# Kernel tuning notes

Hardware: AMD Instinct MI355X
Metric: run time of the kernel (lower is better)

## Reference

```python
import jax, jax.numpy as jnp
import numpy as np

N_NODES = 2048
N_EDGES = 8192
EDGE_DIM = 10
EDGE_HIDDEN = 32
HID = 160


def nnconv(x, edge_index, edge_attr, w1, b1, w2, b2, root, bias):
    """PyG-style NNConv with aggr='mean'.
    x: [N, HID], edge_attr: [E, EDGE_DIM], edge_index: [2, E] (src, dst).
    Per-edge weight W_e = MLP(e) reshaped to [HID, HID]; message = x[src] @ W_e,
    mean-aggregated at dst, plus root transform and bias.
    """
    n = x.shape[0]
    h = jax.nn.relu(edge_attr @ w1 + b1)                     # [E, EDGE_HIDDEN]
    W = (h @ w2 + b2).reshape(-1, HID, HID)                  # [E, HID, HID]
    src, dst = edge_index[0], edge_index[1]
    msg = jnp.einsum('ei,eio->eo', x[src], W)                # [E, HID]
    summed = jax.ops.segment_sum(msg, dst, num_segments=n)   # [N, HID]
    cnt = jax.ops.segment_sum(jnp.ones((msg.shape[0],), x.dtype), dst,
                              num_segments=n)
    aggr = summed / jnp.maximum(cnt, 1.0)[:, None]           # mean; 0 for isolated
    return aggr + x @ root + bias


def setup_inputs() -> dict:
    key = jax.random.key(0)
    ks = jax.random.split(key, 16)
    s = 1.0 / np.sqrt(HID)
    se = 1.0 / np.sqrt(EDGE_DIM)
    sh = 1.0 / np.sqrt(EDGE_HIDDEN)
    inp = {
        'x': jax.random.normal(ks[0], (N_NODES, HID), jnp.float32),
        'edge_attr': jax.random.uniform(ks[1], (N_EDGES, EDGE_DIM), jnp.float32),
        # conv1 (subgraph_conv1) params
        'w1_a': jax.random.normal(ks[2], (EDGE_DIM, EDGE_HIDDEN), jnp.float32) * se,
        'b1_a': jnp.zeros((EDGE_HIDDEN,), jnp.float32),
        'w2_a': jax.random.normal(ks[3], (EDGE_HIDDEN, HID * HID), jnp.float32) * sh,
        'b2_a': jnp.zeros((HID * HID,), jnp.float32),
        'root_a': jax.random.normal(ks[4], (HID, HID), jnp.float32) * s,
        'bias_a': jnp.zeros((HID,), jnp.float32),
        # conv2 (subgraph_conv2, applied twice) params
        'w1_b': jax.random.normal(ks[5], (EDGE_DIM, EDGE_HIDDEN), jnp.float32) * se,
        'b1_b': jnp.zeros((EDGE_HIDDEN,), jnp.float32),
        'w2_b': jax.random.normal(ks[6], (EDGE_HIDDEN, HID * HID), jnp.float32) * sh,
        'b2_b': jnp.zeros((HID * HID,), jnp.float32),
        'root_b': jax.random.normal(ks[7], (HID, HID), jnp.float32) * s,
        'bias_b': jnp.zeros((HID,), jnp.float32),
        'edge_index': jax.random.randint(ks[8], (2, N_EDGES), 0, N_NODES, jnp.int64),
    }
    return inp


def reference(x, edge_attr, w1_a, b1_a, w2_a, b2_a, root_a, bias_a,
              w1_b, b1_b, w2_b, b2_b, root_b, bias_b, edge_index):
    # subgraph_conv1 -> ReLU -> subgraph_conv2 -> ReLU -> subgraph_conv2
    h = jax.nn.relu(nnconv(x, edge_index, edge_attr,
                           w1_a, b1_a, w2_a, b2_a, root_a, bias_a))
    h = jax.nn.relu(nnconv(h, edge_index, edge_attr,
                           w1_b, b1_b, w2_b, b2_b, root_b, bias_b))
    h = nnconv(h, edge_index, edge_attr,
               w1_b, b1_b, w2_b, b2_b, root_b, bias_b)
    return h
```

## Files before the change

kernel.cpp:

```cpp
#include <hip/hip_runtime.h>

#define NN 2048
#define NE 8192
#define ED 10
#define EH 32
#define HID 160
#define KT 5440
#define KS 10
#define KSL 544
#define MT 32
#define APAD 552
#define NNH (NN * HID)

typedef __attribute__((ext_vector_type(8))) short short8;
typedef __attribute__((ext_vector_type(4))) float f32x4;
typedef unsigned int u32;

__device__ __forceinline__ ushort f2bf(float v) {
    u32 u = __float_as_uint(v);
    u += 0x7FFF + ((u >> 16) & 1);
    return (ushort)(u >> 16);
}
__device__ __forceinline__ u32 packbf(float lo, float hi) {
    return ((u32)f2bf(hi) << 16) | f2bf(lo);
}
__device__ __forceinline__ void gl2lds16(const ushort* g, ushort* l) {
    __builtin_amdgcn_global_load_lds(
        (const __attribute__((address_space(1))) u32*)g,
        (__attribute__((address_space(3))) u32*)l, 16, 0, 0);
}

__global__ __launch_bounds__(256) void k_prep(
        const float* __restrict__ ea,
        const float* __restrict__ w1a, const float* __restrict__ b1a,
        const float* __restrict__ w1b, const float* __restrict__ b1b,
        float* __restrict__ ha, float* __restrict__ hb,
        const float* __restrict__ w2a, const float* __restrict__ b2a,
        const float* __restrict__ roota,
        const float* __restrict__ w2b, const float* __restrict__ b2b,
        const float* __restrict__ rootb,
        ushort* __restrict__ WcA, ushort* __restrict__ WcB,
        const float* __restrict__ biasa, const float* __restrict__ biasb,
        float* __restrict__ xacc0, float* __restrict__ xacc1,
        float* __restrict__ outb,
        const int* __restrict__ ei, int* __restrict__ doff,
        int* __restrict__ degg, float* __restrict__ dinv,
        int* __restrict__ delist) {
    __shared__ __align__(16) char smem[21760];
    int b = blockIdx.x, t = threadIdx.x;

    if (b < 512) {
        int set = b >> 8, rel = b & 255;
        const float* w1 = set ? w1b : w1a;
        const float* b1 = set ? b1b : b1a;
        float* h = set ? hb : ha;
        int idx = rel * 1024 + t * 4;
        int e = idx >> 5, j0 = idx & 31;
        float o4[4];
#pragma unroll
        for (int u = 0; u < 4; ++u) {
            float acc = b1[j0 + u];
#pragma unroll
            for (int i = 0; i < ED; ++i) acc += ea[e * ED + i] * w1[i * EH + j0 + u];
            o4[u] = fmaxf(acc, 0.f);
        }
        *(float4*)&h[idx] = *(const float4*)o4;
        return;
    }
    if (b < 672) {
        int rel = b - 512;
        int set = rel / 80, i0 = (rel % 80) * 2;
        u32 (*tile)[34] = (u32(*)[34])smem;
        const float* w2 = set ? w2b : w2a;
        const float* b2 = set ? b2b : b2a;
        const float* root = set ? rootb : roota;
        ushort* W = set ? WcB : WcA;
        if (t < HID) {
#pragma unroll
            for (int di = 0; di < 2; ++di) {
                int i = i0 + di;
#pragma unroll
                for (int p = 0; p < 16; ++p) {
                    float v0 = w2[(size_t)(2 * p) * 25600 + i * HID + t];
                    float v1 = w2[(size_t)(2 * p + 1) * 25600 + i * HID + t];
                    tile[t][di * 17 + p] = packbf(v0, v1);
                }
                tile[t][di * 17 + 16] = packbf(b2[i * HID + t], root[i * HID + t]);
            }
        }
        __syncthreads();
        u32* dst = (u32*)W;
        for (int w = t; w < 5440; w += 256) {
            int o = w / 34, j = w - o * 34;
            dst[(size_t)o * 2720 + i0 * 17 + j] = tile[o][j];
        }
        return;
    }
    if (b < 912) {
        int jb = b - 672;
        int buf = jb / 80, rel = jb % 80;
        float* dst = buf == 0 ? xacc0 : (buf == 1 ? xacc1 : outb);
        const float* bias = buf == 0 ? biasa : biasb;
        int base = rel * 4096 + t * 16;
#pragma unroll
        for (int k = 0; k < 4; ++k) {
            int idx = base + k * 4;
            *(float4*)&dst[idx] = *(const float4*)&bias[idx % HID];
        }
        return;
    }
    int* deg = (int*)smem;
    int* cur = deg + NN;
    int* part = cur + NN;
    for (int i = t; i < NN; i += 256) deg[i] = 0;
    __syncthreads();
    for (int e = t; e < NE; e += 256) atomicAdd(&deg[ei[NE + e]], 1);
    __syncthreads();
    int loc[8], s = 0;
#pragma unroll
    for (int i = 0; i < 8; ++i) { loc[i] = s; s += deg[t * 8 + i]; }
    part[t] = s;
    __syncthreads();
    int tot = s;
    for (int st = 1; st < 256; st <<= 1) {
        int v = (t >= st) ? part[t - st] : 0;
        __syncthreads();
        part[t] += v;
        __syncthreads();
    }
    int base = part[t] - tot;
#pragma unroll
    for (int i = 0; i < 8; ++i) {
        int d = t * 8 + i;
        doff[d] = base + loc[i];
        cur[d] = base + loc[i];
        degg[d] = deg[d];
        dinv[d] = 1.0f / fmaxf((float)deg[d], 1.0f);
    }
    __syncthreads();
    for (int e = t; e < NE; e += 256) {
        int d = ei[NE + e];
        int p = atomicAdd(&cur[d], 1);
        delist[p] = e;
    }
}

__global__ __launch_bounds__(256) void k_layer(
        const float* __restrict__ xin, int dorelu,
        const float* __restrict__ h, const ushort* __restrict__ wc,
        const int* __restrict__ ei, const int* __restrict__ doff,
        const int* __restrict__ degg, const float* __restrict__ dinv,
        const int* __restrict__ delist, float* __restrict__ obuf) {
    __shared__ __align__(16) ushort sA[MT * APAD];
    __shared__ __align__(16) ushort sB[2][160 * 32];
    int t = threadIdx.x;
    int bm = blockIdx.x, ks = blockIdx.y;
    int d0 = bm * MT, i0 = ks * 16;

    auto stage = [&](int buf, int c) {
        size_t k0 = (size_t)ks * KSL + c * 32;
#pragma unroll
        for (int q = 0; q < 2; ++q) {
            int s = t + q * 256;
            int row = s >> 2;
            int lkq = (s & 3) ^ ((row >> 1) & 3);
            gl2lds16(&wc[(size_t)row * KT + k0 + lkq * 8], &sB[buf][s * 8]);
        }
        if (t < 128) {
            int s = t + 512;
            int row = s >> 2;
            int lkq = (s & 3) ^ ((row >> 1) & 3);
            gl2lds16(&wc[(size_t)row * KT + k0 + lkq * 8], &sB[buf][s * 8]);
        }
    };
    stage(0, 0);

    int il = t & 15, i = i0 + il;
    int dA = d0 + (t >> 4), dB = dA + 16;
    auto ldx = [&](int node) {
        float v = xin[node * HID + i];
        return dorelu ? fmaxf(v, 0.f) : v;
    };
    float accA[33], accB[33];
#pragma unroll
    for (int q = 0; q < 33; ++q) { accA[q] = 0.f; accB[q] = 0.f; }

    int aLo = doff[dA], aHi = aLo + degg[dA];
    for (int o = aLo; o < aHi; ++o) {
        int e = delist[o];
        float xs = ldx(ei[e]);
        const float4* hp = (const float4*)&h[(size_t)e * EH];
#pragma unroll
        for (int q8 = 0; q8 < 8; ++q8) {
            float4 hv = hp[q8];
            accA[q8 * 4 + 0] += hv.x * xs;
            accA[q8 * 4 + 1] += hv.y * xs;
            accA[q8 * 4 + 2] += hv.z * xs;
            accA[q8 * 4 + 3] += hv.w * xs;
        }
        accA[32] += xs;
    }
    int bLo = doff[dB], bHi = bLo + degg[dB];
    for (int o = bLo; o < bHi; ++o) {
        int e = delist[o];
        float xs = ldx(ei[e]);
        const float4* hp = (const float4*)&h[(size_t)e * EH];
#pragma unroll
        for (int q8 = 0; q8 < 8; ++q8) {
            float4 hv = hp[q8];
            accB[q8 * 4 + 0] += hv.x * xs;
            accB[q8 * 4 + 1] += hv.y * xs;
            accB[q8 * 4 + 2] += hv.z * xs;
            accB[q8 * 4 + 3] += hv.w * xs;
        }
        accB[32] += xs;
    }
    float rootA = ldx(dA), rootB = ldx(dB);

    {
        float diA = dinv[dA], diB = dinv[dB];
        u32* pa = (u32*)&sA[(t >> 4) * APAD + il * 34];
        u32* pb = (u32*)&sA[((t >> 4) + 16) * APAD + il * 34];
#pragma unroll
        for (int p = 0; p < 16; ++p) {
            pa[p] = packbf(accA[2 * p] * diA, accA[2 * p + 1] * diA);
            pb[p] = packbf(accB[2 * p] * diB, accB[2 * p + 1] * diB);
        }
        pa[16] = packbf(accA[32] * diA, rootA);
        pb[16] = packbf(accB[32] * diB, rootB);
    }
    __syncthreads();

    int wid = t >> 6, lane = t & 63;
    int wm = (wid >> 1) * 16, wn = (wid & 1) * 80;
    int lr = lane & 15, lk = lane >> 4;
    f32x4 acc[5];
#pragma unroll
    for (int j = 0; j < 5; ++j) acc[j] = (f32x4){0.f, 0.f, 0.f, 0.f};

    for (int c = 0; c < 17; ++c) {
        int cur = c & 1;
        if (c + 1 < 17) stage(cur ^ 1, c + 1);
        short8 av = *(const short8*)&sA[(wm + lr) * APAD + c * 32 + lk * 8];
        short8 bv[5];
#pragma unroll
        for (int nt = 0; nt < 5; ++nt) {
            int row = wn + nt * 16 + lr;
            bv[nt] = *(const short8*)&sB[cur][row * 32 +
                                             (lk ^ ((row >> 1) & 3)) * 8];
        }
#pragma unroll
        for (int nt = 0; nt < 5; ++nt)
            acc[nt] = __builtin_amdgcn_mfma_f32_16x16x32_bf16(av, bv[nt], acc[nt], 0, 0, 0);
        __syncthreads();
    }

#pragma unroll
    for (int nt = 0; nt < 5; ++nt) {
        int n = wn + nt * 16 + lr;
        int m0 = d0 + wm + lk * 4;
#pragma unroll
        for (int r = 0; r < 4; ++r)
            unsafeAtomicAdd(&obuf[(size_t)(m0 + r) * HID + n], acc[nt][r]);
    }
}

extern "C" void kernel_launch(void* const* d_in, const int* in_sizes, int n_in,
                              void* d_out, int out_size, void* d_ws, size_t ws_size,
                              hipStream_t stream) {
    const float* x     = (const float*)d_in[0];
    const float* ea    = (const float*)d_in[1];
    const float* w1a   = (const float*)d_in[2];
    const float* b1a   = (const float*)d_in[3];
    const float* w2a   = (const float*)d_in[4];
    const float* b2a   = (const float*)d_in[5];
    const float* roota = (const float*)d_in[6];
    const float* biasa = (const float*)d_in[7];
    const float* w1b   = (const float*)d_in[8];
    const float* b1b   = (const float*)d_in[9];
    const float* w2b   = (const float*)d_in[10];
    const float* b2b   = (const float*)d_in[11];
    const float* rootb = (const float*)d_in[12];
    const float* biasb = (const float*)d_in[13];
    const int*   ei    = (const int*)d_in[14];
    float* out = (float*)d_out;

    char* p = (char*)d_ws;
    float* xacc0 = (float*)p;  p += (size_t)NNH * 4;
    float* xacc1 = (float*)p;  p += (size_t)NNH * 4;
    ushort* WcA  = (ushort*)p; p += (size_t)HID * KT * 2;
    ushort* WcB  = (ushort*)p; p += (size_t)HID * KT * 2;
    float* h_a   = (float*)p;  p += (size_t)NE * EH * 4;
    float* h_b   = (float*)p;  p += (size_t)NE * EH * 4;
    int* doff    = (int*)p;    p += NN * 4;
    int* degg    = (int*)p;    p += NN * 4;
    float* dinv  = (float*)p;  p += NN * 4;
    int* delist  = (int*)p;    p += NE * 4;

    k_prep<<<913, 256, 0, stream>>>(ea, w1a, b1a, w1b, b1b, h_a, h_b,
                                    w2a, b2a, roota, w2b, b2b, rootb, WcA, WcB,
                                    biasa, biasb, xacc0, xacc1, out,
                                    ei, doff, degg, dinv, delist);

    dim3 lg(NN / MT, KS);
    k_layer<<<lg, 256, 0, stream>>>(x, 0, h_a, WcA,
                                    ei, doff, degg, dinv, delist, xacc0);
    k_layer<<<lg, 256, 0, stream>>>(xacc0, 1, h_b, WcB,
                                    ei, doff, degg, dinv, delist, xacc1);
    k_layer<<<lg, 256, 0, stream>>>(xacc1, 1, h_b, WcB,
                                    ei, doff, degg, dinv, delist, out);
}
```

Baseline: 227.3 us.

## Replace atomic split-K output with partial buffers and last-block reduction epilogue

Each split-K block now writes its partial tile to a per-split buffer instead of doing float atomics. A per-row-block counter picks the last-arriving block, which sums the partials, adds the bias, applies ReLU and writes the layer output. This removes the bias-init pass from the prep kernel and the ReLU on loads in the next layer. Other changes: B tiles are read directly from global memory instead of being staged through LDS with double buffering, the edge list stores (edge, src) pairs to drop one indirection, and launch bounds now request 4 blocks per SM. The trade is extra partial-buffer traffic, a fence-and-counter sync, and B loads that are no longer staged through LDS.

New measurement: 474.2 us. 109% more time.

```diff
diff --git a/kernel.cpp b/kernel.cpp
--- a/kernel.cpp
+++ b/kernel.cpp
@@ -24,11 +24,6 @@
 __device__ __forceinline__ u32 packbf(float lo, float hi) {
     return ((u32)f2bf(hi) << 16) | f2bf(lo);
 }
-__device__ __forceinline__ void gl2lds16(const ushort* g, ushort* l) {
-    __builtin_amdgcn_global_load_lds(
-        (const __attribute__((address_space(1))) u32*)g,
-        (__attribute__((address_space(3))) u32*)l, 16, 0, 0);
-}
 
 __global__ __launch_bounds__(256) void k_prep(
         const float* __restrict__ ea,
@@ -40,12 +35,9 @@
         const float* __restrict__ w2b, const float* __restrict__ b2b,
         const float* __restrict__ rootb,
         ushort* __restrict__ WcA, ushort* __restrict__ WcB,
-        const float* __restrict__ biasa, const float* __restrict__ biasb,
-        float* __restrict__ xacc0, float* __restrict__ xacc1,
-        float* __restrict__ outb,
         const int* __restrict__ ei, int* __restrict__ doff,
         int* __restrict__ degg, float* __restrict__ dinv,
-        int* __restrict__ delist) {
+        int2* __restrict__ delist2, int* __restrict__ cnt) {
     __shared__ __align__(16) char smem[21760];
     int b = blockIdx.x, t = threadIdx.x;
 
@@ -96,19 +88,7 @@
         }
         return;
     }
-    if (b < 912) {
-        int jb = b - 672;
-        int buf = jb / 80, rel = jb % 80;
-        float* dst = buf == 0 ? xacc0 : (buf == 1 ? xacc1 : outb);
-        const float* bias = buf == 0 ? biasa : biasb;
-        int base = rel * 4096 + t * 16;
-#pragma unroll
-        for (int k = 0; k < 4; ++k) {
-            int idx = base + k * 4;
-            *(float4*)&dst[idx] = *(const float4*)&bias[idx % HID];
-        }
-        return;
-    }
+    if (t < 64) cnt[t] = 0;
     int* deg = (int*)smem;
     int* cur = deg + NN;
     int* part = cur + NN;
@@ -140,56 +120,36 @@
     __syncthreads();
     for (int e = t; e < NE; e += 256) {
         int d = ei[NE + e];
+        int src = ei[e];
         int p = atomicAdd(&cur[d], 1);
-        delist[p] = e;
-    }
-}
-
-__global__ __launch_bounds__(256) void k_layer(
-        const float* __restrict__ xin, int dorelu,
+        delist2[p] = make_int2(e, src);
+    }
+}
+
+__global__ __launch_bounds__(256, 4) void k_layer(
+        const float* __restrict__ xin,
         const float* __restrict__ h, const ushort* __restrict__ wc,
-        const int* __restrict__ ei, const int* __restrict__ doff,
+        const int2* __restrict__ delist2, const int* __restrict__ doff,
         const int* __restrict__ degg, const float* __restrict__ dinv,
-        const int* __restrict__ delist, float* __restrict__ obuf) {
+        float* __restrict__ Cp, int* __restrict__ cnt,
+        const float* __restrict__ bias, float* __restrict__ xout, int dorelu) {
     __shared__ __align__(16) ushort sA[MT * APAD];
-    __shared__ __align__(16) ushort sB[2][160 * 32];
+    __shared__ int s_old;
     int t = threadIdx.x;
     int bm = blockIdx.x, ks = blockIdx.y;
     int d0 = bm * MT, i0 = ks * 16;
 
-    auto stage = [&](int buf, int c) {
-        size_t k0 = (size_t)ks * KSL + c * 32;
-#pragma unroll
-        for (int q = 0; q < 2; ++q) {
-            int s = t + q * 256;
-            int row = s >> 2;
-            int lkq = (s & 3) ^ ((row >> 1) & 3);
-            gl2lds16(&wc[(size_t)row * KT + k0 + lkq * 8], &sB[buf][s * 8]);
-        }
-        if (t < 128) {
-            int s = t + 512;
-            int row = s >> 2;
-            int lkq = (s & 3) ^ ((row >> 1) & 3);
-            gl2lds16(&wc[(size_t)row * KT + k0 + lkq * 8], &sB[buf][s * 8]);
-        }
-    };
-    stage(0, 0);
-
     int il = t & 15, i = i0 + il;
     int dA = d0 + (t >> 4), dB = dA + 16;
-    auto ldx = [&](int node) {
-        float v = xin[node * HID + i];
-        return dorelu ? fmaxf(v, 0.f) : v;
-    };
     float accA[33], accB[33];
 #pragma unroll
     for (int q = 0; q < 33; ++q) { accA[q] = 0.f; accB[q] = 0.f; }
 
     int aLo = doff[dA], aHi = aLo + degg[dA];
     for (int o = aLo; o < aHi; ++o) {
-        int e = delist[o];
-        float xs = ldx(ei[e]);
-        const float4* hp = (const float4*)&h[(size_t)e * EH];
+        int2 es = delist2[o];
+        float xs = xin[es.y * HID + i];
+        const float4* hp = (const float4*)&h[(size_t)es.x * EH];
 #pragma unroll
         for (int q8 = 0; q8 < 8; ++q8) {
             float4 hv = hp[q8];
@@ -202,9 +162,9 @@
     }
     int bLo = doff[dB], bHi = bLo + degg[dB];
     for (int o = bLo; o < bHi; ++o) {
-        int e = delist[o];
-        float xs = ldx(ei[e]);
-        const float4* hp = (const float4*)&h[(size_t)e * EH];
+        int2 es = delist2[o];
+        float xs = xin[es.y * HID + i];
+        const float4* hp = (const float4*)&h[(size_t)es.x * EH];
 #pragma unroll
         for (int q8 = 0; q8 < 8; ++q8) {
             float4 hv = hp[q8];
@@ -215,7 +175,7 @@
         }
         accB[32] += xs;
     }
-    float rootA = ldx(dA), rootB = ldx(dB);
+    float rootA = xin[dA * HID + i], rootB = xin[dB * HID + i];
 
     {
         float diA = dinv[dA], diB = dinv[dB];
@@ -238,30 +198,55 @@
 #pragma unroll
     for (int j = 0; j < 5; ++j) acc[j] = (f32x4){0.f, 0.f, 0.f, 0.f};
 
+    const ushort* wb = wc + (size_t)ks * KSL + lk * 8;
+#pragma unroll
     for (int c = 0; c < 17; ++c) {
-        int cur = c & 1;
-        if (c + 1 < 17) stage(cur ^ 1, c + 1);
         short8 av = *(const short8*)&sA[(wm + lr) * APAD + c * 32 + lk * 8];
         short8 bv[5];
 #pragma unroll
         for (int nt = 0; nt < 5; ++nt) {
             int row = wn + nt * 16 + lr;
-            bv[nt] = *(const short8*)&sB[cur][row * 32 +
-                                             (lk ^ ((row >> 1) & 3)) * 8];
+            bv[nt] = *(const short8*)&wb[(size_t)row * KT + c * 32];
         }
 #pragma unroll
         for (int nt = 0; nt < 5; ++nt)
             acc[nt] = __builtin_amdgcn_mfma_f32_16x16x32_bf16(av, bv[nt], acc[nt], 0, 0, 0);
-        __syncthreads();
-    }
-
+    }
+
+    float* Cb = Cp + (size_t)ks * NNH;
 #pragma unroll
     for (int nt = 0; nt < 5; ++nt) {
         int n = wn + nt * 16 + lr;
         int m0 = d0 + wm + lk * 4;
 #pragma unroll
         for (int r = 0; r < 4; ++r)
-            unsafeAtomicAdd(&obuf[(size_t)(m0 + r) * HID + n], acc[nt][r]);
+            Cb[(size_t)(m0 + r) * HID + n] = acc[nt][r];
+    }
+
+    __threadfence();
+    __syncthreads();
+    if (t == 0) s_old = atomicAdd(&cnt[bm], 1);
+    __syncthreads();
+    if (s_old == KS - 1) {
+        __threadfence();
+#pragma unroll
+        for (int j = 0; j < 5; ++j) {
+            int f4 = j * 256 + t;
+            int node = d0 + f4 / 40;
+            int o = (f4 % 40) * 4;
+            float4 s = *(const float4*)&bias[o];
+#pragma unroll
+            for (int p = 0; p < KS; ++p) {
+                float4 v = *(const float4*)&Cp[(size_t)p * NNH + node * HID + o];
+                s.x += v.x; s.y += v.y; s.z += v.z; s.w += v.w;
+            }
+            if (dorelu) {
+                s.x = fmaxf(s.x, 0.f); s.y = fmaxf(s.y, 0.f);
+                s.z = fmaxf(s.z, 0.f); s.w = fmaxf(s.w, 0.f);
+            }
+            *(float4*)&xout[node * HID + o] = s;
+        }
+        if (t == 0) cnt[bm] = 0;
     }
 }
 
@@ -286,6 +271,7 @@
     float* out = (float*)d_out;
 
     char* p = (char*)d_ws;
+    float* Cp    = (float*)p;  p += (size_t)KS * NNH * 4;
     float* xacc0 = (float*)p;  p += (size_t)NNH * 4;
     float* xacc1 = (float*)p;  p += (size_t)NNH * 4;
     ushort* WcA  = (ushort*)p; p += (size_t)HID * KT * 2;
@@ -295,18 +281,18 @@
     int* doff    = (int*)p;    p += NN * 4;
     int* degg    = (int*)p;    p += NN * 4;
     float* dinv  = (float*)p;  p += NN * 4;
-    int* delist  = (int*)p;    p += NE * 4;
-
-    k_prep<<<913, 256, 0, stream>>>(ea, w1a, b1a, w1b, b1b, h_a, h_b,
+    int2* delist2 = (int2*)p;  p += NE * 8;
+    int* cnt     = (int*)p;    p += 64 * 4;
+
+    k_prep<<<673, 256, 0, stream>>>(ea, w1a, b1a, w1b, b1b, h_a, h_b,
                                     w2a, b2a, roota, w2b, b2b, rootb, WcA, WcB,
-                                    biasa, biasb, xacc0, xacc1, out,
-                                    ei, doff, degg, dinv, delist);
+                                    ei, doff, degg, dinv, delist2, cnt);
 
     dim3 lg(NN / MT, KS);
-    k_layer<<<lg, 256, 0, stream>>>(x, 0, h_a, WcA,
-                                    ei, doff, degg, dinv, delist, xacc0);
-    k_layer<<<lg, 256, 0, stream>>>(xacc0, 1, h_b, WcB,
-                                    ei, doff, degg, dinv, delist, xacc1);
-    k_layer<<<lg, 256, 0, stream>>>(xacc1, 1, h_b, WcB,
-                                    ei, doff, degg, dinv, delist, out);
-}
+    k_layer<<<lg, 256, 0, stream>>>(x, h_a, WcA, delist2, doff, degg, dinv,
+                                    Cp, cnt, biasa, xacc0, 1);
+    k_layer<<<lg, 256, 0, stream>>>(xacc0, h_b, WcB, delist2, doff, degg, dinv,
+                                    Cp, cnt, biasb, xacc1, 1);
+    k_layer<<<lg, 256, 0, stream>>>(xacc1, h_b, WcB, delist2, doff, degg, dinv,
+                                    Cp, cnt, biasb, out, 0);
+}
```
